# Kernel optimization log

Measured on AMD Instinct MI355X. Metric: run time of the kernel, lower is better.

Reference implementation:

```python
import jax, jax.numpy as jnp
import numpy as np

H, D = 16, 64  # heads, dim_head


def _rope(x):
    # x: (b, h, n, d). rotary-embedding-torch style: interleaved pairs, theta=10000.
    n, d = x.shape[-2], x.shape[-1]
    inv_freq = 1.0 / (10000.0 ** (jnp.arange(0, d, 2, dtype=jnp.float32) / d))  # (d/2,)
    ang = jnp.arange(n, dtype=jnp.float32)[:, None] * inv_freq[None, :]  # (n, d/2)
    cos = jnp.repeat(jnp.cos(ang), 2, axis=-1).astype(x.dtype)  # (n, d) interleaved
    sin = jnp.repeat(jnp.sin(ang), 2, axis=-1).astype(x.dtype)
    xp = x.reshape(*x.shape[:-1], d // 2, 2)
    rot = jnp.stack((-xp[..., 1], xp[..., 0]), axis=-1).reshape(x.shape)
    return x * cos + rot * sin


def setup_inputs() -> dict:
    key = jax.random.key(0)
    k1, k2, k3 = jax.random.split(key, 3)
    b, n, dim = 2, 2048, 1024
    inner = H * D
    x = jax.random.normal(k1, (b, n, dim), jnp.float32)
    w_qkv = jax.random.normal(k2, (dim, 3 * inner), jnp.float32) / np.sqrt(dim).astype(np.float32)
    w_out = jax.random.normal(k3, (inner, dim), jnp.float32) / np.sqrt(inner).astype(np.float32)
    b_out = jnp.zeros((dim,), jnp.float32)
    return {"x": x, "w_qkv": w_qkv, "w_out": w_out, "b_out": b_out}


def reference(x, w_qkv, w_out, b_out):
    b, n, _ = x.shape
    qkv = x @ w_qkv  # (b, n, 3*H*D)
    q, k, v = jnp.split(qkv, 3, axis=-1)

    def split_heads(t):
        return t.reshape(b, n, H, D).transpose(0, 2, 1, 3)  # (b, h, n, d)

    q, k, v = split_heads(q), split_heads(k), split_heads(v)
    q = _rope(q)
    k = _rope(k)
    scale = 1.0 / jnp.sqrt(jnp.asarray(D, dtype=x.dtype))
    scores = jnp.einsum('bhqd,bhkd->bhqk', q, k) * scale
    attn = jax.nn.softmax(scores, axis=-1)
    o = jnp.einsum('bhqk,bhkd->bhqd', attn, v)
    o = o.transpose(0, 2, 1, 3).reshape(b, n, H * D)
    return o @ w_out + b_out
```

## Files before the change

kernel.cpp:

```cpp
#include <hip/hip_runtime.h>
#include <math.h>

#define B_    2
#define N_    2048
#define DIM_  1024
#define H_    16
#define D_    64
#define INNER_ 1024
#define QKVC_ 3072

typedef __attribute__((ext_vector_type(8))) short short8;
typedef __attribute__((ext_vector_type(4))) short short4v;
typedef __attribute__((ext_vector_type(4))) float f32x4;
typedef __attribute__((ext_vector_type(4))) float float4v;
typedef _Float16 half8 __attribute__((ext_vector_type(8)));
typedef __fp16 fp16v2 __attribute__((ext_vector_type(2)));

union h8u { short8 s; half8 h; fp16v2 h2[4]; };
static __device__ __forceinline__ half8 s2h(short8 s) { h8u u; u.s = s; return u.h; }

static __device__ __forceinline__ unsigned short f2h(float f) {
    _Float16 h = (_Float16)f;
    unsigned short u;
    __builtin_memcpy(&u, &h, 2);
    return u;
}

static __device__ __forceinline__ void gload16(const void* g, void* l) {
    __builtin_amdgcn_global_load_lds((__attribute__((address_space(1))) void*)(g),
                                     (__attribute__((address_space(3))) void*)(l),
                                     16, 0, 0);
}

__global__ __launch_bounds__(256) void convert_all(const float* __restrict__ X,
                                                   const float* __restrict__ Wq,
                                                   const float* __restrict__ Wo,
                                                   unsigned short* __restrict__ Xh,
                                                   unsigned short* __restrict__ WqT,
                                                   unsigned short* __restrict__ WoT) {
    __shared__ unsigned short Sh[64][65];
    const int blk = blockIdx.x;
    const int tid = threadIdx.x;
    if (blk < 2048) {
        int t = blk * 256 + tid;
        size_t off = (size_t)t * 8;
        float4v a = *(const float4v*)(X + off);
        float4v b = *(const float4v*)(X + off + 4);
        short8 o;
#pragma unroll
        for (int j = 0; j < 4; ++j) {
            o[j]     = (short)f2h(a[j]);
            o[4 + j] = (short)f2h(b[j]);
        }
        *(short8*)(Xh + off) = o;
        return;
    }
    const float* W;
    unsigned short* T;
    int n0, k0, Nw;
    if (blk < 2816) {
        int g = blk - 2048;
        W = Wq; T = WqT; Nw = QKVC_;
        n0 = (g % 48) * 64; k0 = (g / 48) * 64;
    } else {
        int g = blk - 2816;
        W = Wo; T = WoT; Nw = DIM_;
        n0 = (g % 16) * 64; k0 = (g / 16) * 64;
    }
#pragma unroll
    for (int l = 0; l < 16; ++l) {
        int idx = tid + l * 256;
        int r = idx >> 6, c = idx & 63;
        Sh[c][r] = f2h(W[(size_t)(k0 + r) * Nw + n0 + c]);
    }
    __syncthreads();
#pragma unroll
    for (int l = 0; l < 16; ++l) {
        int idx = tid + l * 256;
        int r = idx >> 6, c = idx & 63;
        T[(size_t)(n0 + r) * 1024 + k0 + c] = Sh[r][c];
    }
}

#define GEMM_STAGE_H(gA, gB)                                                       \
    {                                                                              \
        int rr0 = w * 32 + (lane >> 2), rr1 = w * 32 + 16 + (lane >> 2);           \
        int kc = (lane & 3) * 8;                                                   \
        gload16(gA + (size_t)(m0 + rr0) * 1024 + k0 + kc, sA + (w * 32) * 32);     \
        gload16(gA + (size_t)(m0 + rr1) * 1024 + k0 + kc, sA + (w * 32 + 16) * 32);\
        gload16(gB + (size_t)(n0 + rr0) * 1024 + k0 + kc, sB + (w * 32) * 32);     \
        gload16(gB + (size_t)(n0 + rr1) * 1024 + k0 + kc, sB + (w * 32 + 16) * 32);\
    }

#define GEMM_BODY_H()                                                              \
    half8 af[4], bf[4];                                                            \
    _Pragma("unroll") for (int f = 0; f < 4; ++f) {                                \
        af[f] = s2h(*(const short8*)&sA[(wr + f * 16 + (lane & 15)) * 32 + (lane >> 4) * 8]); \
        bf[f] = s2h(*(const short8*)&sB[(wc + f * 16 + (lane & 15)) * 32 + (lane >> 4) * 8]); \
    }                                                                              \
    _Pragma("unroll") for (int i = 0; i < 4; ++i)                                  \
        _Pragma("unroll") for (int j = 0; j < 4; ++j)                              \
            acc[i][j] = __builtin_amdgcn_mfma_f32_16x16x32_f16(af[i], bf[j], acc[i][j], 0, 0, 0);

#define QSCALE 0.180336879963f
__global__ __launch_bounds__(256) void qkv_gemm_mfma(const unsigned short* __restrict__ Ah,
                                                     const unsigned short* __restrict__ Bh,
                                                     unsigned short* __restrict__ Qh,
                                                     unsigned short* __restrict__ Kh,
                                                     unsigned short* __restrict__ Vh) {
    __shared__ __align__(16) unsigned short sA[4096], sB[4096];
    const int tid = threadIdx.x;
    const int lane = tid & 63, w = tid >> 6;
    const int wr = (w >> 1) * 64, wc = (w & 1) * 64;
    const int m0 = blockIdx.y * 128, n0 = blockIdx.x * 128;
    f32x4 acc[4][4] = {};

    for (int k0 = 0; k0 < 1024; k0 += 32) {
        GEMM_STAGE_H(Ah, Bh);
        __syncthreads();
        GEMM_BODY_H();
        __syncthreads();
    }

    const int seg = n0 >> 10;
    const int parity = lane & 1;

#pragma unroll
    for (int i = 0; i < 4; ++i) {
        int mbase = m0 + wr + i * 16 + (lane >> 4) * 4;
#pragma unroll
        for (int j = 0; j < 4; ++j) {
            int col = n0 + wc + j * 16 + (lane & 15);
            int wcol = col & 1023;
            int h = wcol >> 6, dd = wcol & 63;
            unsigned short* dst = (seg == 0) ? Qh : (seg == 1 ? Kh : Vh);
            if (seg == 2) {
#pragma unroll
                for (int r = 0; r < 4; ++r) {
                    int row = mbase + r;
                    int b = row >> 11, n = row & (N_ - 1);
                    dst[((size_t)(b * H_ + h) * N_ + n) * D_ + dd] = f2h(acc[i][j][r]);
                }
            } else {
                float freq = __builtin_amdgcn_exp2f((float)(dd >> 1) * -0.4152410118f);
#pragma unroll
                for (int r = 0; r < 4; ++r) {
                    int row = mbase + r;
                    int b = row >> 11, n = row & (N_ - 1);
                    float ang = (float)n * freq;
                    float s = __sinf(ang);
                    float c = __cosf(ang);
                    float val = acc[i][j][r];
                    float partner = __shfl_xor(val, 1);
                    float rot = parity ? (val * c + partner * s)
                                       : (val * c - partner * s);
                    if (seg == 0) rot *= QSCALE;
                    dst[((size_t)(b * H_ + h) * N_ + n) * D_ + dd] = f2h(rot);
                }
            }
        }
    }
}

__global__ __launch_bounds__(256) void out_gemm_mfma(const unsigned short* __restrict__ Ah,
                                                     const unsigned short* __restrict__ Bh,
                                                     const float* __restrict__ bias,
                                                     float* __restrict__ C) {
    __shared__ __align__(16) unsigned short sA[4096], sB[4096];
    const int tid = threadIdx.x;
    const int lane = tid & 63, w = tid >> 6;
    const int wr = (w >> 1) * 64, wc = (w & 1) * 64;
    const int m0 = blockIdx.y * 128, n0 = blockIdx.x * 128;
    f32x4 acc[4][4] = {};

    for (int k0 = 0; k0 < 1024; k0 += 32) {
        GEMM_STAGE_H(Ah, Bh);
        __syncthreads();
        GEMM_BODY_H();
        __syncthreads();
    }

#pragma unroll
    for (int i = 0; i < 4; ++i) {
        int mbase = m0 + wr + i * 16 + (lane >> 4) * 4;
#pragma unroll
        for (int j = 0; j < 4; ++j) {
            int col = n0 + wc + j * 16 + (lane & 15);
            float bv = bias[col];
#pragma unroll
            for (int r = 0; r < 4; ++r)
                C[(size_t)(mbase + r) * DIM_ + col] = acc[i][j][r] + bv;
        }
    }
}

#define PADV 72
#define NT   (N_ / 64)
#define RESC_THR 8.0f
__global__ __launch_bounds__(512, 4) void attn_mfma(const unsigned short* __restrict__ Qh,
                                                    const unsigned short* __restrict__ Kh,
                                                    const unsigned short* __restrict__ Vh,
                                                    unsigned short* __restrict__ Oh) {
    __shared__ __align__(16) unsigned short Ks[2 * 64 * 64];
    __shared__ __align__(16) unsigned short Vt[2][64][PADV];
    const int tid = threadIdx.x;
    const int w = tid >> 6;
    const int l = tid & 63;
    const int lr = l & 15, lg = l >> 4;

    const int f = blockIdx.y * gridDim.x + blockIdx.x;
    const int x = f & 7, g = f >> 3;
    const int bh = x * 4 + (g >> 4);
    const int q0 = (g & 15) * 128;
    const size_t base = (size_t)bh * N_ * D_;

    const int srow = tid >> 3;
    const int scg  = tid & 7;
    const int gcg  = scg ^ (srow & 7);
    const unsigned short* ksrc = Kh + base + (size_t)srow * D_ + gcg * 8;
    unsigned short* kdst = Ks + w * 512;

    const int kb0 = lr * 64 + (lg ^ (lr & 7)) * 8;
    const int kb1 = lr * 64 + ((lg + 4) ^ (lr & 7)) * 8;

    const int sd0 = (tid & 15) * 4;
    const int skv = (tid >> 4) * 2;
    const int vpos = ((skv >> 5) * 32) + (((skv >> 2) & 3) * 8) +
                     (((skv >> 4) & 1) * 4) + (skv & 3);

    const unsigned short* qrow = Qh + base + (size_t)(q0 + w * 16 + lr) * D_ + lg * 8;
    const half8 qf0 = s2h(*(const short8*)qrow);
    const half8 qf1 = s2h(*(const short8*)(qrow + 32));

    f32x4 oacc[4] = {};
    float mrow = -1e30f, lsum = 0.f;

    gload16(ksrc, kdst);
    {
        short4v r0 = *(const short4v*)(Vh + base + (size_t)(skv + 0) * D_ + sd0);
        short4v r1 = *(const short4v*)(Vh + base + (size_t)(skv + 1) * D_ + sd0);
#pragma unroll
        for (int j = 0; j < 4; ++j) {
            unsigned int pk = (unsigned int)(unsigned short)r0[j] |
                              ((unsigned int)(unsigned short)r1[j] << 16);
            *(unsigned int*)&Vt[0][sd0 + j][vpos] = pk;
        }
    }

    for (int ti = 0; ti < NT; ++ti) {
        const int cur = ti & 1, nxt = cur ^ 1;
        __syncthreads();

        short4v n0v = {}, n1v = {};
        if (ti + 1 < NT) {
            gload16(ksrc + (size_t)(ti + 1) * 64 * D_, kdst + nxt * 4096);
            const unsigned short* nsrc = Vh + base + (size_t)((ti + 1) * 64 + skv) * D_ + sd0;
            n0v = *(const short4v*)nsrc;
            n1v = *(const short4v*)(nsrc + D_);
        }

        f32x4 sacc[4] = {};
        const unsigned short* kbuf = Ks + cur * 4096;
        __builtin_amdgcn_s_setprio(1);
#pragma unroll
        for (int t = 0; t < 4; ++t) {
            half8 kf0 = s2h(*(const short8*)(kbuf + t * 1024 + kb0));
            half8 kf1 = s2h(*(const short8*)(kbuf + t * 1024 + kb1));
            sacc[t] = __builtin_amdgcn_mfma_f32_16x16x32_f16(kf0, qf0, sacc[t], 0, 0, 0);
            sacc[t] = __builtin_amdgcn_mfma_f32_16x16x32_f16(kf1, qf1, sacc[t], 0, 0, 0);
        }
        __builtin_amdgcn_s_setprio(0);

        float tm0 = fmaxf(fmaxf(sacc[0][0], sacc[0][1]), fmaxf(sacc[0][2], sacc[0][3]));
        float tm1 = fmaxf(fmaxf(sacc[1][0], sacc[1][1]), fmaxf(sacc[1][2], sacc[1][3]));
        float tm2 = fmaxf(fmaxf(sacc[2][0], sacc[2][1]), fmaxf(sacc[2][2], sacc[2][3]));
        float tm3 = fmaxf(fmaxf(sacc[3][0], sacc[3][1]), fmaxf(sacc[3][2], sacc[3][3]));
        float tm = fmaxf(fmaxf(tm0, tm1), fmaxf(tm2, tm3));
        tm = fmaxf(tm, __shfl_xor(tm, 16));
        tm = fmaxf(tm, __shfl_xor(tm, 32));

        if (!__all(tm - mrow <= RESC_THR)) {
            float nm = fmaxf(mrow, tm);
            float al = __builtin_amdgcn_exp2f(mrow - nm);
            mrow = nm;
            lsum *= al;
#pragma unroll
            for (int r = 0; r < 4; ++r) {
                float alq = __shfl(al, lg * 4 + r);
#pragma unroll
                for (int dt = 0; dt < 4; ++dt) oacc[dt][r] *= alq;
            }
        }

        h8u pu[2];
#pragma unroll
        for (int t = 0; t < 4; ++t) {
            float e0 = __builtin_amdgcn_exp2f(sacc[t][0] - mrow);
            float e1 = __builtin_amdgcn_exp2f(sacc[t][1] - mrow);
            float e2 = __builtin_amdgcn_exp2f(sacc[t][2] - mrow);
            float e3 = __builtin_amdgcn_exp2f(sacc[t][3] - mrow);
            lsum += (e0 + e1) + (e2 + e3);
            pu[t >> 1].h2[(t & 1) * 2]     = __builtin_amdgcn_cvt_pkrtz(e0, e1);
            pu[t >> 1].h2[(t & 1) * 2 + 1] = __builtin_amdgcn_cvt_pkrtz(e2, e3);
        }

        __builtin_amdgcn_s_setprio(1);
#pragma unroll
        for (int m2 = 0; m2 < 2; ++m2)
#pragma unroll
            for (int dt = 0; dt < 4; ++dt) {
                half8 vf = s2h(*(const short8*)&Vt[cur][dt * 16 + lr][m2 * 32 + lg * 8]);
                oacc[dt] = __builtin_amdgcn_mfma_f32_16x16x32_f16(pu[m2].h, vf, oacc[dt], 0, 0, 0);
            }
        __builtin_amdgcn_s_setprio(0);

        if (ti + 1 < NT) {
#pragma unroll
            for (int j = 0; j < 4; ++j) {
                unsigned int pk = (unsigned int)(unsigned short)n0v[j] |
                                  ((unsigned int)(unsigned short)n1v[j] << 16);
                *(unsigned int*)&Vt[nxt][sd0 + j][vpos] = pk;
            }
        }
    }

    lsum += __shfl_xor(lsum, 16);
    lsum += __shfl_xor(lsum, 32);
    int b = bh >> 4, h = bh & 15;
#pragma unroll
    for (int r = 0; r < 4; ++r) {
        float ls = __shfl(lsum, lg * 4 + r);
        float inv = 1.0f / ls;
        size_t orow = ((size_t)b * N_ + q0 + w * 16 + lg * 4 + r) * INNER_ + h * 64 + lr;
#pragma unroll
        for (int dt = 0; dt < 4; ++dt)
            Oh[orow + 16 * dt] = f2h(oacc[dt][r] * inv);
    }
}

extern "C" void kernel_launch(void* const* d_in, const int* in_sizes, int n_in,
                              void* d_out, int out_size, void* d_ws, size_t ws_size,
                              hipStream_t stream) {
    const float* x     = (const float*)d_in[0];
    const float* w_qkv = (const float*)d_in[1];
    const float* w_out = (const float*)d_in[2];
    const float* b_out = (const float*)d_in[3];
    float* out = (float*)d_out;

    unsigned short* Xh  = (unsigned short*)d_ws;
    unsigned short* WqT = Xh + 4194304;
    unsigned short* WoT = WqT + 3145728;
    unsigned short* Qh  = WoT + 1048576;
    unsigned short* Kh  = Qh + 4194304;
    unsigned short* Vh  = Kh + 4194304;

    convert_all<<<dim3(3072), 256, 0, stream>>>(x, w_qkv, w_out, Xh, WqT, WoT);
    qkv_gemm_mfma<<<dim3(QKVC_ / 128, 32), 256, 0, stream>>>(Xh, WqT, Qh, Kh, Vh);
    attn_mfma<<<dim3(N_ / 128, B_ * H_), 512, 0, stream>>>(Qh, Kh, Vh, Xh);
    out_gemm_mfma<<<dim3(DIM_ / 128, 32), 256, 0, stream>>>(Xh, WoT, b_out, out);
}
```

Baseline: 133.9 us.

## Software-pipeline attention PV MFMA one tile behind QK with triple-buffered V

Restructures the attention loop so the P·V matrix multiply for the previous key tile is issued right after the current tile's QK^T MFMAs, letting softmax exp work overlap with MFMA execution. The V tile in shared memory becomes triple-buffered with rotating read/current/write indices, and the deferred rescale of the output accumulator is applied before the delayed PV step. A final epilogue drains the last tile. This adds LDS usage and register pressure (carried P fragments and flags), which may reduce occupancy at the 4-blocks-per-CU launch bound.

Result: no change. 131.6 us (-1.7%).

```diff
diff --git a/kernel.cpp b/kernel.cpp
--- a/kernel.cpp
+++ b/kernel.cpp
@@ -202,7 +202,7 @@
                                                     const unsigned short* __restrict__ Vh,
                                                     unsigned short* __restrict__ Oh) {
     __shared__ __align__(16) unsigned short Ks[2 * 64 * 64];
-    __shared__ __align__(16) unsigned short Vt[2][64][PADV];
+    __shared__ __align__(16) unsigned short Vt[3][64][PADV];
     const int tid = threadIdx.x;
     const int w = tid >> 6;
     const int l = tid & 63;
@@ -234,6 +234,11 @@
 
     f32x4 oacc[4] = {};
     float mrow = -1e30f, lsum = 0.f;
+    h8u pa_prev[2];
+    pa_prev[0].s = short8{0,0,0,0,0,0,0,0};
+    pa_prev[1].s = short8{0,0,0,0,0,0,0,0};
+    float al_prev = 1.f;
+    bool resc_prev = false;
 
     gload16(ksrc, kdst);
     {
@@ -247,20 +252,22 @@
         }
     }
 
+    int rd = 2, cu = 0, wr_ = 1;
+
     for (int ti = 0; ti < NT; ++ti) {
-        const int cur = ti & 1, nxt = cur ^ 1;
+        const int kcur = ti & 1, knxt = kcur ^ 1;
         __syncthreads();
 
         short4v n0v = {}, n1v = {};
         if (ti + 1 < NT) {
-            gload16(ksrc + (size_t)(ti + 1) * 64 * D_, kdst + nxt * 4096);
+            gload16(ksrc + (size_t)(ti + 1) * 64 * D_, kdst + knxt * 4096);
             const unsigned short* nsrc = Vh + base + (size_t)((ti + 1) * 64 + skv) * D_ + sd0;
             n0v = *(const short4v*)nsrc;
             n1v = *(const short4v*)(nsrc + D_);
         }
 
         f32x4 sacc[4] = {};
-        const unsigned short* kbuf = Ks + cur * 4096;
+        const unsigned short* kbuf = Ks + kcur * 4096;
         __builtin_amdgcn_s_setprio(1);
 #pragma unroll
         for (int t = 0; t < 4; ++t) {
@@ -268,6 +275,23 @@
             half8 kf1 = s2h(*(const short8*)(kbuf + t * 1024 + kb1));
             sacc[t] = __builtin_amdgcn_mfma_f32_16x16x32_f16(kf0, qf0, sacc[t], 0, 0, 0);
             sacc[t] = __builtin_amdgcn_mfma_f32_16x16x32_f16(kf1, qf1, sacc[t], 0, 0, 0);
+        }
+        if (ti > 0) {
+            if (resc_prev) {
+#pragma unroll
+                for (int r = 0; r < 4; ++r) {
+                    float alq = __shfl(al_prev, lg * 4 + r);
+#pragma unroll
+                    for (int dt = 0; dt < 4; ++dt) oacc[dt][r] *= alq;
+                }
+            }
+#pragma unroll
+            for (int m2 = 0; m2 < 2; ++m2)
+#pragma unroll
+                for (int dt = 0; dt < 4; ++dt) {
+                    half8 vf = s2h(*(const short8*)&Vt[rd][dt * 16 + lr][m2 * 32 + lg * 8]);
+                    oacc[dt] = __builtin_amdgcn_mfma_f32_16x16x32_f16(pa_prev[m2].h, vf, oacc[dt], 0, 0, 0);
+                }
         }
         __builtin_amdgcn_s_setprio(0);
 
@@ -284,15 +308,12 @@
             float al = __builtin_amdgcn_exp2f(mrow - nm);
             mrow = nm;
             lsum *= al;
-#pragma unroll
-            for (int r = 0; r < 4; ++r) {
-                float alq = __shfl(al, lg * 4 + r);
-#pragma unroll
-                for (int dt = 0; dt < 4; ++dt) oacc[dt][r] *= alq;
-            }
-        }
-
-        h8u pu[2];
+            al_prev = al;
+            resc_prev = true;
+        } else {
+            resc_prev = false;
+        }
+
 #pragma unroll
         for (int t = 0; t < 4; ++t) {
             float e0 = __builtin_amdgcn_exp2f(sacc[t][0] - mrow);
@@ -300,29 +321,36 @@
             float e2 = __builtin_amdgcn_exp2f(sacc[t][2] - mrow);
             float e3 = __builtin_amdgcn_exp2f(sacc[t][3] - mrow);
             lsum += (e0 + e1) + (e2 + e3);
-            pu[t >> 1].h2[(t & 1) * 2]     = __builtin_amdgcn_cvt_pkrtz(e0, e1);
-            pu[t >> 1].h2[(t & 1) * 2 + 1] = __builtin_amdgcn_cvt_pkrtz(e2, e3);
-        }
-
-        __builtin_amdgcn_s_setprio(1);
-#pragma unroll
-        for (int m2 = 0; m2 < 2; ++m2)
-#pragma unroll
-            for (int dt = 0; dt < 4; ++dt) {
-                half8 vf = s2h(*(const short8*)&Vt[cur][dt * 16 + lr][m2 * 32 + lg * 8]);
-                oacc[dt] = __builtin_amdgcn_mfma_f32_16x16x32_f16(pu[m2].h, vf, oacc[dt], 0, 0, 0);
-            }
-        __builtin_amdgcn_s_setprio(0);
+            pa_prev[t >> 1].h2[(t & 1) * 2]     = __builtin_amdgcn_cvt_pkrtz(e0, e1);
+            pa_prev[t >> 1].h2[(t & 1) * 2 + 1] = __builtin_amdgcn_cvt_pkrtz(e2, e3);
+        }
 
         if (ti + 1 < NT) {
 #pragma unroll
             for (int j = 0; j < 4; ++j) {
                 unsigned int pk = (unsigned int)(unsigned short)n0v[j] |
                                   ((unsigned int)(unsigned short)n1v[j] << 16);
-                *(unsigned int*)&Vt[nxt][sd0 + j][vpos] = pk;
+                *(unsigned int*)&Vt[wr_][sd0 + j][vpos] = pk;
             }
         }
-    }
+        int t_ = rd; rd = cu; cu = wr_; wr_ = t_;
+    }
+
+    if (resc_prev) {
+#pragma unroll
+        for (int r = 0; r < 4; ++r) {
+            float alq = __shfl(al_prev, lg * 4 + r);
+#pragma unroll
+            for (int dt = 0; dt < 4; ++dt) oacc[dt][r] *= alq;
+        }
+    }
+#pragma unroll
+    for (int m2 = 0; m2 < 2; ++m2)
+#pragma unroll
+        for (int dt = 0; dt < 4; ++dt) {
+            half8 vf = s2h(*(const short8*)&Vt[rd][dt * 16 + lr][m2 * 32 + lg * 8]);
+            oacc[dt] = __builtin_amdgcn_mfma_f32_16x16x32_f16(pa_prev[m2].h, vf, oacc[dt], 0, 0, 0);
+        }
 
     lsum += __shfl_xor(lsum, 16);
     lsum += __shfl_xor(lsum, 32);
```
